# Kernel tuning notes

Measured on AMD Instinct MI355X. Metric: run time of the kernel, lower is better.

Reference implementation:

```python
import jax, jax.numpy as jnp
import numpy as np
from jax import lax

BS, K, N = 8, 8, 16            # batch, gathers per sample, picks per curve
T, WG = 3072, 64               # gather time samples, traces
H, WC = 256, 256               # CVEncoder ScaleSize
RH, RW = 1024, 512             # resize (also GatherEncoder outLen=RH)
T0, T1 = 0.0, 7000.0           # tInt[0], tInt[-1]


def setup_inputs() -> dict:
    key = jax.random.key(0)
    ks = jax.random.split(key, 8)
    gather = jax.random.normal(ks[0], (BS, K, T, WG), jnp.float32)
    # cv: times sorted, strictly > 0, within [T0, T1]; velocities within VMM range
    times = jnp.sort(jax.random.uniform(ks[1], (BS, K, N), minval=100.0, maxval=T1), axis=-1)
    vels = jnp.sort(jax.random.uniform(ks[2], (BS, K, N), minval=1500.0, maxval=4500.0), axis=-1)
    cv = jnp.stack([times, vels], axis=-1).astype(jnp.float32)
    VMM = jnp.tile(jnp.array([1500.0, 4500.0], jnp.float32), (BS, 1))
    def cw(k, shape):
        return (jax.random.normal(k, shape, jnp.float32) * 0.1)
    params = dict(
        w1=cw(ks[3], (1, 1, 3, 3)), b1=jnp.zeros((1,), jnp.float32), g1=jnp.ones((1,), jnp.float32), be1=jnp.zeros((1,), jnp.float32),
        w2=cw(ks[4], (2, 3, 3, 3)), b2=jnp.zeros((2,), jnp.float32), g2=jnp.ones((2,), jnp.float32), be2=jnp.zeros((2,), jnp.float32),
        w3=cw(ks[5], (1, 2, 3, 2)), b3=jnp.zeros((1,), jnp.float32), g3=jnp.ones((1,), jnp.float32), be3=jnp.zeros((1,), jnp.float32),
        wf=cw(ks[6], (1, 1, 3, 3)), bf=jnp.zeros((1,), jnp.float32), gf=jnp.ones((1,), jnp.float32), bef=jnp.zeros((1,), jnp.float32),
    )
    return {"gather": gather, "cv": cv, "VMM": VMM, **params}


def _conv(x, w, b, stride, pad):
    y = lax.conv_general_dilated(x, w, stride, pad, dimension_numbers=("NCHW", "OIHW", "NCHW"))
    return y + b[None, :, None, None]


def _bn(x, g, b, eps=1e-5):
    # training-mode BatchNorm2d: stats over (N, H, W)
    m = jnp.mean(x, (0, 2, 3), keepdims=True)
    v = jnp.var(x, (0, 2, 3), keepdims=True)
    return (x - m) / jnp.sqrt(v + eps) * g[None, :, None, None] + b[None, :, None, None]


def _lrelu(x):
    return jnp.where(x >= 0, x, 0.1 * x)


def _cbl(x, w, b, g, be, stride):
    return _lrelu(_bn(_conv(x, w, b, stride, "VALID"), g, be))


def _maxpool(x, k):
    p = k // 2
    return lax.reduce_window(x, -jnp.inf, lax.max, (1, 1, k, k), (1, 1, 1, 1),
                             ((0, 0), (0, 0), (p, p), (p, p)))


def _cv_mask(cv, VMM):
    # normalize times to fractional row index and velocities to fractional col index
    dt = (T1 - T0) / (H - 1)
    t_idx = (cv[..., 0] - T0) / dt                                        # (BS,K,N)
    dv = (VMM[:, 1] - VMM[:, 0]) / (WC - 1)                               # (BS,)
    v_idx = (cv[..., 1] - VMM[:, 0, None, None]) / dv[:, None, None]      # (BS,K,N)
    t_flat = t_idx.reshape(-1, N)
    v_flat = v_idx.reshape(-1, N)
    tq = jnp.arange(H, dtype=jnp.float32)
    # per-curve piecewise-linear interpolation of v over the time grid
    v_curve = jax.vmap(lambda xp, fp: jnp.interp(tq, xp, fp))(t_flat, v_flat)  # (M,H)
    v_int = jnp.clip(v_curve.astype(jnp.int32), 0, WC - 1)
    M = BS * K
    mask = jnp.full((M, H, WC), 0.01, jnp.float32)
    mask = mask.at[jnp.arange(M)[:, None], jnp.arange(H)[None, :], v_int].add(0.9)
    mask = mask.reshape(BS, K, H, WC)
    # bilinear resize, half-pixel centers == torch align_corners=False
    return jax.image.resize(mask, (BS, K, RH, RW), method="linear")


def _forward(gather, cv, VMM, w1, b1, g1, be1, w2, b2, g2, be2, w3, b3, g3, be3, wf, bf, gf, bef):
    cv_mask = lax.stop_gradient(_cv_mask(cv, VMM))          # CVEncoder runs under no_grad
    x = gather.reshape(-1, 1, T, WG)                        # (BS*K,1,T,WG)
    x = x / jnp.max(jnp.abs(x))                             # mode='mute': keep sign
    x = _cbl(x, w1, b1, g1, be1, (3, 2))                    # (M,1,1024,31)
    xcat = jnp.concatenate([x, _maxpool(x, 3), _maxpool(x, 5)], axis=1)
    x = _cbl(xcat, w2, b2, g2, be2, (3, 2))                 # (M,2,341,15)
    x = _cbl(x, w3, b3, g3, be3, (3, 2))                    # (M,1,113,7)
    x = jax.image.resize(x, (x.shape[0], 1, RH, 1), method="linear")
    genr = x.reshape(BS, K, RH, 1)
    mix = jnp.sum(genr * cv_mask, axis=1, keepdims=True)    # (BS,1,RH,RW)
    y = _conv(mix, wf, bf, (1, 1), ((1, 1), (1, 1)))
    return _lrelu(_bn(y, gf, bef))


def reference(gather, cv, VMM, w1, b1, g1, be1, w2, b2, g2, be2, w3, b3, g3, be3, wf, bf, gf, bef):
    return _forward(gather, cv, VMM, w1, b1, g1, be1, w2, b2, g2, be2, w3, b3, g3, be3, wf, bf, gf, bef)
```

## Files before the change

kernel.cpp:

```cpp
#include <hip/hip_runtime.h>
#include <math.h>

#define BSZ 8
#define KG  8
#define NP  16
#define MM  64
#define TT  3072
#define WGN 64
#define HH  256
#define WCN 256
#define RHN 1024
#define RWN 512

#define C1H 1024
#define C1W 31
#define C2H 341
#define C2W 15
#define C3H 113
#define C3W 7

#define N_GATHER (MM*TT*WGN)
#define N1 (MM*C1H*C1W)
#define N2 (MM*C2H*C2W)
#define N3 (MM*C3H*C3W)
#define NF (BSZ*RHN*RWN)

#define SL 8

#define OFF_AMAX 640
#define OFF_SCAL 672
#define OFF_VINT 768
#define OFF_Y1   (OFF_VINT + MM*HH*4)
#define OFF_Y2   (OFF_Y1  + N1*4)
#define OFF_Y3   (OFF_Y2  + 2*N2*4)
#define OFF_GENR (OFF_Y3  + N3*4)

__device__ __forceinline__ void blockAdd2(double s, double ss, double* o0, double* o1) {
    __shared__ double red[4][2];
    __syncthreads();
    int lane = threadIdx.x & 63, wid = threadIdx.x >> 6;
#pragma unroll
    for (int off = 32; off > 0; off >>= 1) {
        s  += __shfl_down(s,  off, 64);
        ss += __shfl_down(ss, off, 64);
    }
    if (lane == 0) { red[wid][0] = s; red[wid][1] = ss; }
    __syncthreads();
    if (threadIdx.x == 0) {
        double a = 0, b = 0;
        int nw = blockDim.x >> 6;
        for (int i = 0; i < nw; i++) { a += red[i][0]; b += red[i][1]; }
        int slot = blockIdx.x & (SL - 1);
        atomicAdd(&o0[slot], a); atomicAdd(&o1[slot], b);
    }
}

__global__ void k_absmax(const float* __restrict__ g, unsigned int* amax) {
    __shared__ float red[4];
    int tid = blockIdx.x * blockDim.x + threadIdx.x;
    int stride = gridDim.x * blockDim.x;
    const float4* g4 = (const float4*)g;
    float m = 0.f;
    for (int i = tid; i < N_GATHER / 4; i += stride) {
        float4 v = g4[i];
        m = fmaxf(m, fmaxf(fmaxf(fabsf(v.x), fabsf(v.y)), fmaxf(fabsf(v.z), fabsf(v.w))));
    }
#pragma unroll
    for (int off = 32; off > 0; off >>= 1) m = fmaxf(m, __shfl_down(m, off, 64));
    int lane = threadIdx.x & 63, wid = threadIdx.x >> 6;
    if (lane == 0) red[wid] = m;
    __syncthreads();
    if (threadIdx.x == 0) {
        float mm = fmaxf(fmaxf(red[0], red[1]), fmaxf(red[2], red[3]));
        atomicMax(&amax[blockIdx.x & (SL - 1)], __float_as_uint(mm));
    }
}

__global__ void k_conv1(const float* __restrict__ g, const float* __restrict__ w1,
                        const float* __restrict__ b1, const unsigned int* __restrict__ amax,
                        float* __restrict__ y1, double* sums) {
    float mx = 0.f;
#pragma unroll
    for (int i = 0; i < SL; i++) mx = fmaxf(mx, __uint_as_float(amax[i]));
    float inv = 1.0f / mx;
    float w[9];
#pragma unroll
    for (int i = 0; i < 9; i++) w[i] = w1[i] * inv;
    float bb = b1[0];
    double s = 0, ss = 0;
    int stride = gridDim.x * blockDim.x;
    for (int idx = blockIdx.x * blockDim.x + threadIdx.x; idx < N1; idx += stride) {
        int ow = idx % C1W;
        int t2 = idx / C1W;
        int oh = t2 % C1H;
        int m  = t2 / C1H;
        const float* xp = g + (size_t)m * TT * WGN + (size_t)(oh * 3) * WGN + ow * 2;
        float acc = bb;
#pragma unroll
        for (int r = 0; r < 3; r++)
#pragma unroll
            for (int c = 0; c < 3; c++) acc += w[r * 3 + c] * xp[r * WGN + c];
        y1[idx] = acc;
        s += acc; ss += (double)acc * (double)acc;
    }
    blockAdd2(s, ss, &sums[0], &sums[SL]);
}

__global__ void k_bnfin(const double* __restrict__ s, const float* __restrict__ g,
                        const float* __restrict__ be, float* __restrict__ ab,
                        int nch, double n) {
    int c = threadIdx.x;
    if (c < nch) {
        double sum = 0, sumsq = 0;
        for (int j = 0; j < SL; j++) {
            sum   += s[(2 * c) * SL + j];
            sumsq += s[(2 * c + 1) * SL + j];
        }
        double mean = sum / n;
        double var  = sumsq / n - mean * mean;
        double a = (double)g[c] / sqrt(var + 1e-5);
        ab[2 * c]     = (float)a;
        ab[2 * c + 1] = (float)((double)be[c] - mean * a);
    }
}

#define F2_OH 32
#define F2_NCH 11
#define F2_NRMAX (3*F2_OH + 4)
__global__ void k_fused2(const float* __restrict__ y1, const float* __restrict__ scal,
                         const float* __restrict__ w2, const float* __restrict__ b2,
                         float* __restrict__ y2, double* sums) {
    __shared__ float sact[F2_NRMAX][32];
    __shared__ float sr3[F2_NRMAX][32];
    __shared__ float sr5[F2_NRMAX][32];
    int m   = blockIdx.x / F2_NCH;
    int ch  = blockIdx.x % F2_NCH;
    int oh0 = ch * F2_OH;
    int OHa = min(F2_OH, C2H - oh0);
    int NR  = 3 * OHa + 4;
    int gl0 = 3 * oh0 - 2;
    float a1 = scal[0], b1 = scal[1];
    const float* yp = y1 + (size_t)m * C1H * C1W;
    for (int i = threadIdx.x; i < NR * C1W; i += blockDim.x) {
        int l = i / C1W, w = i % C1W;
        int gr = gl0 + l;
        float v = -INFINITY;
        if (gr >= 0 && gr < C1H) {
            v = a1 * yp[gr * C1W + w] + b1;
            v = v >= 0.f ? v : 0.1f * v;
        }
        sact[l][w] = v;
    }
    __syncthreads();
    for (int i = threadIdx.x; i < NR * C1W; i += blockDim.x) {
        int l = i / C1W, w = i % C1W;
        int wl1 = max(w - 1, 0), wr1 = min(w + 1, C1W - 1);
        int wl2 = max(w - 2, 0), wr2 = min(w + 2, C1W - 1);
        float c  = sact[l][w];
        float m3 = fmaxf(fmaxf(sact[l][wl1], c), sact[l][wr1]);
        float m5 = fmaxf(fmaxf(m3, sact[l][wl2]), sact[l][wr2]);
        sr3[l][w] = m3;
        sr5[l][w] = m5;
    }
    __syncthreads();
    double s0 = 0, ss0 = 0, s1 = 0, ss1 = 0;
    for (int o = threadIdx.x; o < OHa * C2W; o += blockDim.x) {
        int lo = o / C2W, ow = o % C2W;
        float a0 = b2[0], acc1 = b2[1];
#pragma unroll
        for (int i = 0; i < 3; i++) {
            int l = 3 * lo + 2 + i;
#pragma unroll
            for (int j = 0; j < 3; j++) {
                int wc = 2 * ow + j;
                float v0 = sact[l][wc];
                float v1 = fmaxf(fmaxf(sr3[l - 1][wc], sr3[l][wc]), sr3[l + 1][wc]);
                float v2 = fmaxf(fmaxf(fmaxf(sr5[l - 2][wc], sr5[l - 1][wc]), sr5[l][wc]),
                                 fmaxf(sr5[l + 1][wc], sr5[l + 2][wc]));
                int ki = i * 3 + j;
                a0   += w2[ki] * v0 + w2[9 + ki] * v1 + w2[18 + ki] * v2;
                acc1 += w2[27 + ki] * v0 + w2[36 + ki] * v1 + w2[45 + ki] * v2;
            }
        }
        size_t ob = (size_t)m * (2 * C2H * C2W) + (size_t)(oh0 + lo) * C2W + ow;
        y2[ob] = a0;
        y2[ob + C2H * C2W] = acc1;
        s0 += a0; ss0 += (double)a0 * a0;
        s1 += acc1; ss1 += (double)acc1 * acc1;
    }
    blockAdd2(s0, ss0, &sums[2 * SL], &sums[3 * SL]);
    blockAdd2(s1, ss1, &sums[4 * SL], &sums[5 * SL]);
}

__global__ void k_conv3(const float* __restrict__ y2, const float* __restrict__ scal,
                        const float* __restrict__ w3, const float* __restrict__ b3,
                        float* __restrict__ y3, double* sums) {
    double s = 0, ss = 0;
    float a20 = scal[2], b20 = scal[3], a21 = scal[4], b21 = scal[5];
    int stride = gridDim.x * blockDim.x;
    for (int idx = blockIdx.x * blockDim.x + threadIdx.x; idx < N3; idx += stride) {
        int ow = idx % C3W;
        int t2 = idx / C3W;
        int oh = t2 % C3H;
        int m  = t2 / C3H;
        float acc = b3[0];
#pragma unroll
        for (int i = 0; i < 2; i++) {
            float aa = i ? a21 : a20, bb = i ? b21 : b20;
            const float* cp = y2 + (size_t)m * (2 * C2H * C2W) + (size_t)i * C2H * C2W
                              + (size_t)(oh * 3) * C2W + ow * 2;
#pragma unroll
            for (int r = 0; r < 3; r++)
#pragma unroll
                for (int c = 0; c < 2; c++) {
                    float v = aa * cp[r * C2W + c] + bb;
                    v = v >= 0.f ? v : 0.1f * v;
                    acc += w3[i * 6 + r * 2 + c] * v;
                }
        }
        y3[idx] = acc;
        s += acc; ss += (double)acc * acc;
    }
    blockAdd2(s, ss, &sums[6 * SL], &sums[7 * SL]);
}

__global__ void k_vint(const float* __restrict__ cv, const float* __restrict__ VMM,
                       int* __restrict__ vint) {
    __shared__ float tt[NP], vv[NP];
    int m = blockIdx.x;
    int b = m >> 3;
    if (threadIdx.x < NP) {
        int n = threadIdx.x;
        float t = cv[(m * NP + n) * 2 + 0];
        float v = cv[(m * NP + n) * 2 + 1];
        float dt = 7000.0f / 255.0f;
        tt[n] = t / dt;
        float vmin = VMM[b * 2], vmax = VMM[b * 2 + 1];
        float dv = (vmax - vmin) / 255.0f;
        vv[n] = (v - vmin) / dv;
    }
    __syncthreads();
    int h = threadIdx.x;
    float x = (float)h;
    float val;
    if (x <= tt[0]) val = vv[0];
    else if (x >= tt[NP - 1]) val = vv[NP - 1];
    else {
        int i = 1;
        while (i < NP - 1 && tt[i] <= x) i++;
        float d = tt[i] - tt[i - 1];
        val = (d != 0.f) ? vv[i - 1] + (x - tt[i - 1]) / d * (vv[i] - vv[i - 1]) : vv[i];
    }
    int vi = (int)val;
    vi = max(0, min(WCN - 1, vi));
    vint[m * HH + h] = vi;
}

__global__ void k_genr(const float* __restrict__ y3, const float* __restrict__ scal,
                       float* __restrict__ genr) {
    __shared__ float tile[C3H * C3W];
    int m = blockIdx.x;
    float a = scal[6], b = scal[7];
    for (int i = threadIdx.x; i < C3H * C3W; i += blockDim.x) {
        float v = a * y3[m * C3H * C3W + i] + b;
        tile[i] = v >= 0.f ? v : 0.1f * v;
    }
    __syncthreads();
    const float cw0 = 4.f / 37.f, cw1 = 5.f / 37.f, cw2 = 6.f / 37.f, cw3 = 7.f / 37.f;
    const float cw[7] = { cw0, cw1, cw2, cw3, cw2, cw1, cw0 };
    for (int i = threadIdx.x; i < RHN; i += blockDim.x) {
        float sh = (i + 0.5f) * (113.0f / 1024.0f) - 0.5f;
        float fl = floorf(sh);
        float fr = sh - fl;
        int i0 = (int)fl, i1 = i0 + 1;
        i0 = max(0, min(C3H - 1, i0));
        i1 = max(0, min(C3H - 1, i1));
        float acc = 0.f;
#pragma unroll
        for (int x = 0; x < 7; x++) {
            float v = (1.f - fr) * tile[i0 * C3W + x] + fr * tile[i1 * C3W + x];
            acc += cw[x] * v;
        }
        genr[m * RHN + i] = acc;
    }
}

#define MC_TH 16
__global__ void k_mixconvf(const float* __restrict__ genr, const int* __restrict__ vint,
                           const float* __restrict__ wf, const float* __restrict__ bf,
                           float* __restrict__ out, double* sums) {
    __shared__ float tile[MC_TH + 2][RWN + 2];
    __shared__ float Grow[MC_TH + 2];
    int b  = blockIdx.x / (RHN / MC_TH);
    int chk = blockIdx.x % (RHN / MC_TH);
    int h0 = chk * MC_TH;
    for (int i = threadIdx.x; i < (MC_TH + 2) * (RWN + 2); i += blockDim.x)
        ((float*)tile)[i] = 0.f;
    if (threadIdx.x < MC_TH + 2) Grow[threadIdx.x] = 0.f;
    __syncthreads();
    if (threadIdx.x < (MC_TH + 2) * KG) {
        int r = threadIdx.x / KG, k = threadIdx.x % KG;
        int h = h0 - 1 + r;
        if (h >= 0 && h < RHN) {
            int m = b * KG + k;
            float g = genr[m * RHN + h];
            atomicAdd(&Grow[r], g);
            float sh = (h + 0.5f) * 0.25f - 0.5f;
            float fl = floorf(sh);
            float fh = sh - fl;
            int ih0 = (int)fl, ih1 = ih0 + 1;
            ih0 = max(0, min(HH - 1, ih0));
            ih1 = max(0, min(HH - 1, ih1));
            int vv[2] = { vint[m * HH + ih0], vint[m * HH + ih1] };
            float aa[2] = { 0.9f * g * (1.f - fh), 0.9f * g * fh };
#pragma unroll
            for (int t = 0; t < 2; t++) {
                int v = vv[t]; float A = aa[t];
                if (v == 0) {
                    atomicAdd(&tile[r][1 + 0], A);
                    atomicAdd(&tile[r][1 + 1], 0.75f * A);
                    atomicAdd(&tile[r][1 + 2], 0.25f * A);
                } else if (v == WCN - 1) {
                    atomicAdd(&tile[r][1 + 509], 0.25f * A);
                    atomicAdd(&tile[r][1 + 510], 0.75f * A);
                    atomicAdd(&tile[r][1 + 511], A);
                } else {
                    atomicAdd(&tile[r][1 + 2 * v - 1], 0.25f * A);
                    atomicAdd(&tile[r][1 + 2 * v],     0.75f * A);
                    atomicAdd(&tile[r][1 + 2 * v + 1], 0.75f * A);
                    atomicAdd(&tile[r][1 + 2 * v + 2], 0.25f * A);
                }
            }
        }
    }
    __syncthreads();
    for (int i = threadIdx.x; i < (MC_TH + 2) * RWN; i += blockDim.x) {
        int r = i / RWN, w = i % RWN;
        int h = h0 - 1 + r;
        if (h >= 0 && h < RHN) tile[r][w + 1] += 0.01f * Grow[r];
    }
    __syncthreads();
    float w[9];
#pragma unroll
    for (int i = 0; i < 9; i++) w[i] = wf[i];
    float bb = bf[0];
    double s = 0, ss = 0;
    for (int o = threadIdx.x; o < MC_TH * RWN; o += blockDim.x) {
        int lr = o / RWN, x = o % RWN;
        float acc = bb;
#pragma unroll
        for (int dr = 0; dr < 3; dr++)
#pragma unroll
            for (int dc = 0; dc < 3; dc++)
                acc += w[dr * 3 + dc] * tile[lr + dr][x + dc];
        out[((size_t)b * RHN + (h0 + lr)) * RWN + x] = acc;
        s += acc; ss += (double)acc * acc;
    }
    blockAdd2(s, ss, &sums[8 * SL], &sums[9 * SL]);
}

__global__ void k_act4(float4* __restrict__ x, const float* __restrict__ ab, int n4) {
    int i = blockIdx.x * blockDim.x + threadIdx.x;
    if (i < n4) {
        float a = ab[0], b = ab[1];
        float4 v = x[i];
        v.x = a * v.x + b; v.x = v.x >= 0.f ? v.x : 0.1f * v.x;
        v.y = a * v.y + b; v.y = v.y >= 0.f ? v.y : 0.1f * v.y;
        v.z = a * v.z + b; v.z = v.z >= 0.f ? v.z : 0.1f * v.z;
        v.w = a * v.w + b; v.w = v.w >= 0.f ? v.w : 0.1f * v.w;
        x[i] = v;
    }
}

extern "C" void kernel_launch(void* const* d_in, const int* in_sizes, int n_in,
                              void* d_out, int out_size, void* d_ws, size_t ws_size,
                              hipStream_t stream) {
    const float* gather = (const float*)d_in[0];
    const float* cv     = (const float*)d_in[1];
    const float* VMM    = (const float*)d_in[2];
    const float* w1 = (const float*)d_in[3];
    const float* b1 = (const float*)d_in[4];
    const float* g1 = (const float*)d_in[5];
    const float* be1 = (const float*)d_in[6];
    const float* w2 = (const float*)d_in[7];
    const float* b2 = (const float*)d_in[8];
    const float* g2 = (const float*)d_in[9];
    const float* be2 = (const float*)d_in[10];
    const float* w3 = (const float*)d_in[11];
    const float* b3 = (const float*)d_in[12];
    const float* g3 = (const float*)d_in[13];
    const float* be3 = (const float*)d_in[14];
    const float* wf = (const float*)d_in[15];
    const float* bf = (const float*)d_in[16];
    const float* gf = (const float*)d_in[17];
    const float* bef = (const float*)d_in[18];
    float* out = (float*)d_out;

    char* ws = (char*)d_ws;
    double* sums        = (double*)ws;
    unsigned int* amax  = (unsigned int*)(ws + OFF_AMAX);
    float* scal         = (float*)(ws + OFF_SCAL);
    int*   vint         = (int*)(ws + OFF_VINT);
    float* y1           = (float*)(ws + OFF_Y1);
    float* y2           = (float*)(ws + OFF_Y2);
    float* y3           = (float*)(ws + OFF_Y3);
    float* genr         = (float*)(ws + OFF_GENR);

    hipMemsetAsync(d_ws, 0, 768, stream);

    k_absmax<<<512, 256, 0, stream>>>(gather, amax);
    k_conv1<<<512, 256, 0, stream>>>(gather, w1, b1, amax, y1, sums);
    k_bnfin<<<1, 64, 0, stream>>>(sums + 0, g1, be1, scal + 0, 1, (double)N1);
    k_fused2<<<MM * F2_NCH, 256, 0, stream>>>(y1, scal, w2, b2, y2, sums);
    k_bnfin<<<1, 64, 0, stream>>>(sums + 2 * SL, g2, be2, scal + 2, 2, (double)N2);
    k_conv3<<<198, 256, 0, stream>>>(y2, scal, w3, b3, y3, sums);
    k_bnfin<<<1, 64, 0, stream>>>(sums + 6 * SL, g3, be3, scal + 6, 1, (double)N3);
    k_vint<<<MM, 256, 0, stream>>>(cv, VMM, vint);
    k_genr<<<MM, 256, 0, stream>>>(y3, scal, genr);
    k_mixconvf<<<BSZ * (RHN / MC_TH), 256, 0, stream>>>(genr, vint, wf, bf, out, sums);
    k_bnfin<<<1, 64, 0, stream>>>(sums + 8 * SL, gf, bef, scal + 8, 1, (double)NF);
    k_act4<<<(NF / 4 + 255) / 256, 256, 0, stream>>>((float4*)out, scal + 8, NF / 4);
}
```

Baseline: 205.8 us.

## Drop absmax pass via BN scale invariance, fold BN finalize into consumers

Removes the global abs-max reduction over the gather tensor. Training-mode BatchNorm after conv1 cancels any uniform input scaling, apart from the small eps term, so that pass is redundant. The separate BN-finalize kernels are replaced by an inline helper that each consumer kernel runs from the atomic sums. The final in-place activation pass is removed by splitting the mix/conv stage into a statistics pass and a second pass that recomputes the tile and writes the normalized, activated output directly. This trades extra compute in the mix stage for fewer launches and less full-tensor memory traffic.

```diff
diff --git a/kernel.cpp b/kernel.cpp
--- a/kernel.cpp
+++ b/kernel.cpp
@@ -19,7 +19,6 @@
 #define C3H 113
 #define C3W 7
 
-#define N_GATHER (MM*TT*WGN)
 #define N1 (MM*C1H*C1W)
 #define N2 (MM*C2H*C2W)
 #define N3 (MM*C3H*C3W)
@@ -27,8 +26,6 @@
 
 #define SL 8
 
-#define OFF_AMAX 640
-#define OFF_SCAL 672
 #define OFF_VINT 768
 #define OFF_Y1   (OFF_VINT + MM*HH*4)
 #define OFF_Y2   (OFF_Y1  + N1*4)
@@ -55,37 +52,27 @@
     }
 }
 
-__global__ void k_absmax(const float* __restrict__ g, unsigned int* amax) {
-    __shared__ float red[4];
-    int tid = blockIdx.x * blockDim.x + threadIdx.x;
-    int stride = gridDim.x * blockDim.x;
-    const float4* g4 = (const float4*)g;
-    float m = 0.f;
-    for (int i = tid; i < N_GATHER / 4; i += stride) {
-        float4 v = g4[i];
-        m = fmaxf(m, fmaxf(fmaxf(fabsf(v.x), fabsf(v.y)), fmaxf(fabsf(v.z), fabsf(v.w))));
-    }
-#pragma unroll
-    for (int off = 32; off > 0; off >>= 1) m = fmaxf(m, __shfl_down(m, off, 64));
-    int lane = threadIdx.x & 63, wid = threadIdx.x >> 6;
-    if (lane == 0) red[wid] = m;
-    __syncthreads();
-    if (threadIdx.x == 0) {
-        float mm = fmaxf(fmaxf(red[0], red[1]), fmaxf(red[2], red[3]));
-        atomicMax(&amax[blockIdx.x & (SL - 1)], __float_as_uint(mm));
-    }
+__device__ __forceinline__ float2 bn_ab(const double* __restrict__ sums, int c,
+                                        const float* __restrict__ g,
+                                        const float* __restrict__ be, double n) {
+    double sum = 0, sumsq = 0;
+#pragma unroll
+    for (int j = 0; j < SL; j++) {
+        sum   += sums[(2 * c) * SL + j];
+        sumsq += sums[(2 * c + 1) * SL + j];
+    }
+    double mean = sum / n;
+    double var  = sumsq / n - mean * mean;
+    double a = (double)g[c] / sqrt(var + 1e-5);
+    return make_float2((float)a, (float)((double)be[c] - mean * a));
 }
 
 __global__ void k_conv1(const float* __restrict__ g, const float* __restrict__ w1,
-                        const float* __restrict__ b1, const unsigned int* __restrict__ amax,
+                        const float* __restrict__ b1,
                         float* __restrict__ y1, double* sums) {
-    float mx = 0.f;
-#pragma unroll
-    for (int i = 0; i < SL; i++) mx = fmaxf(mx, __uint_as_float(amax[i]));
-    float inv = 1.0f / mx;
     float w[9];
 #pragma unroll
-    for (int i = 0; i < 9; i++) w[i] = w1[i] * inv;
+    for (int i = 0; i < 9; i++) w[i] = w1[i];
     float bb = b1[0];
     double s = 0, ss = 0;
     int stride = gridDim.x * blockDim.x;
@@ -106,47 +93,30 @@
     blockAdd2(s, ss, &sums[0], &sums[SL]);
 }
 
-__global__ void k_bnfin(const double* __restrict__ s, const float* __restrict__ g,
-                        const float* __restrict__ be, float* __restrict__ ab,
-                        int nch, double n) {
-    int c = threadIdx.x;
-    if (c < nch) {
-        double sum = 0, sumsq = 0;
-        for (int j = 0; j < SL; j++) {
-            sum   += s[(2 * c) * SL + j];
-            sumsq += s[(2 * c + 1) * SL + j];
-        }
-        double mean = sum / n;
-        double var  = sumsq / n - mean * mean;
-        double a = (double)g[c] / sqrt(var + 1e-5);
-        ab[2 * c]     = (float)a;
-        ab[2 * c + 1] = (float)((double)be[c] - mean * a);
-    }
-}
-
 #define F2_OH 32
 #define F2_NCH 11
 #define F2_NRMAX (3*F2_OH + 4)
-__global__ void k_fused2(const float* __restrict__ y1, const float* __restrict__ scal,
+__global__ void k_fused2(const float* __restrict__ y1, const double* __restrict__ sums_r,
+                         const float* __restrict__ g1, const float* __restrict__ be1,
                          const float* __restrict__ w2, const float* __restrict__ b2,
                          float* __restrict__ y2, double* sums) {
     __shared__ float sact[F2_NRMAX][32];
     __shared__ float sr3[F2_NRMAX][32];
     __shared__ float sr5[F2_NRMAX][32];
+    float2 ab1 = bn_ab(sums_r, 0, g1, be1, (double)N1);
     int m   = blockIdx.x / F2_NCH;
     int ch  = blockIdx.x % F2_NCH;
     int oh0 = ch * F2_OH;
     int OHa = min(F2_OH, C2H - oh0);
     int NR  = 3 * OHa + 4;
     int gl0 = 3 * oh0 - 2;
-    float a1 = scal[0], b1 = scal[1];
     const float* yp = y1 + (size_t)m * C1H * C1W;
     for (int i = threadIdx.x; i < NR * C1W; i += blockDim.x) {
         int l = i / C1W, w = i % C1W;
         int gr = gl0 + l;
         float v = -INFINITY;
         if (gr >= 0 && gr < C1H) {
-            v = a1 * yp[gr * C1W + w] + b1;
+            v = ab1.x * yp[gr * C1W + w] + ab1.y;
             v = v >= 0.f ? v : 0.1f * v;
         }
         sact[l][w] = v;
@@ -192,11 +162,13 @@
     blockAdd2(s1, ss1, &sums[4 * SL], &sums[5 * SL]);
 }
 
-__global__ void k_conv3(const float* __restrict__ y2, const float* __restrict__ scal,
+__global__ void k_conv3(const float* __restrict__ y2, const double* __restrict__ sums_r,
+                        const float* __restrict__ g2, const float* __restrict__ be2,
                         const float* __restrict__ w3, const float* __restrict__ b3,
                         float* __restrict__ y3, double* sums) {
+    float2 ab20 = bn_ab(sums_r + 2 * SL, 0, g2, be2, (double)N2);
+    float2 ab21 = bn_ab(sums_r + 2 * SL, 1, g2, be2, (double)N2);
     double s = 0, ss = 0;
-    float a20 = scal[2], b20 = scal[3], a21 = scal[4], b21 = scal[5];
     int stride = gridDim.x * blockDim.x;
     for (int idx = blockIdx.x * blockDim.x + threadIdx.x; idx < N3; idx += stride) {
         int ow = idx % C3W;
@@ -206,7 +178,7 @@
         float acc = b3[0];
 #pragma unroll
         for (int i = 0; i < 2; i++) {
-            float aa = i ? a21 : a20, bb = i ? b21 : b20;
+            float aa = i ? ab21.x : ab20.x, bb = i ? ab21.y : ab20.y;
             const float* cp = y2 + (size_t)m * (2 * C2H * C2W) + (size_t)i * C2H * C2W
                               + (size_t)(oh * 3) * C2W + ow * 2;
 #pragma unroll
@@ -224,11 +196,15 @@
     blockAdd2(s, ss, &sums[6 * SL], &sums[7 * SL]);
 }
 
-__global__ void k_vint(const float* __restrict__ cv, const float* __restrict__ VMM,
-                       int* __restrict__ vint) {
+__global__ void k_vintgenr(const float* __restrict__ cv, const float* __restrict__ VMM,
+                           const float* __restrict__ y3, const double* __restrict__ sums_r,
+                           const float* __restrict__ g3, const float* __restrict__ be3,
+                           int* __restrict__ vint, float* __restrict__ genr) {
     __shared__ float tt[NP], vv[NP];
+    __shared__ float tile[C3H * C3W];
     int m = blockIdx.x;
     int b = m >> 3;
+    float2 ab3 = bn_ab(sums_r + 6 * SL, 0, g3, be3, (double)N3);
     if (threadIdx.x < NP) {
         int n = threadIdx.x;
         float t = cv[(m * NP + n) * 2 + 0];
@@ -239,33 +215,26 @@
         float dv = (vmax - vmin) / 255.0f;
         vv[n] = (v - vmin) / dv;
     }
-    __syncthreads();
-    int h = threadIdx.x;
-    float x = (float)h;
-    float val;
-    if (x <= tt[0]) val = vv[0];
-    else if (x >= tt[NP - 1]) val = vv[NP - 1];
-    else {
-        int i = 1;
-        while (i < NP - 1 && tt[i] <= x) i++;
-        float d = tt[i] - tt[i - 1];
-        val = (d != 0.f) ? vv[i - 1] + (x - tt[i - 1]) / d * (vv[i] - vv[i - 1]) : vv[i];
-    }
-    int vi = (int)val;
-    vi = max(0, min(WCN - 1, vi));
-    vint[m * HH + h] = vi;
-}
-
-__global__ void k_genr(const float* __restrict__ y3, const float* __restrict__ scal,
-                       float* __restrict__ genr) {
-    __shared__ float tile[C3H * C3W];
-    int m = blockIdx.x;
-    float a = scal[6], b = scal[7];
     for (int i = threadIdx.x; i < C3H * C3W; i += blockDim.x) {
-        float v = a * y3[m * C3H * C3W + i] + b;
+        float v = ab3.x * y3[m * C3H * C3W + i] + ab3.y;
         tile[i] = v >= 0.f ? v : 0.1f * v;
     }
     __syncthreads();
+    {
+        int h = threadIdx.x;
+        float x = (float)h;
+        float val;
+        if (x <= tt[0]) val = vv[0];
+        else if (x >= tt[NP - 1]) val = vv[NP - 1];
+        else {
+            int i = 1;
+            while (i < NP - 1 && tt[i] <= x) i++;
+            float d = tt[i] - tt[i - 1];
+            val = (d != 0.f) ? vv[i - 1] + (x - tt[i - 1]) / d * (vv[i] - vv[i - 1]) : vv[i];
+        }
+        int vi = (int)val;
+        vint[m * HH + h] = max(0, min(WCN - 1, vi));
+    }
     const float cw0 = 4.f / 37.f, cw1 = 5.f / 37.f, cw2 = 6.f / 37.f, cw3 = 7.f / 37.f;
     const float cw[7] = { cw0, cw1, cw2, cw3, cw2, cw1, cw0 };
     for (int i = threadIdx.x; i < RHN; i += blockDim.x) {
@@ -286,14 +255,10 @@
 }
 
 #define MC_TH 16
-__global__ void k_mixconvf(const float* __restrict__ genr, const int* __restrict__ vint,
-                           const float* __restrict__ wf, const float* __restrict__ bf,
-                           float* __restrict__ out, double* sums) {
-    __shared__ float tile[MC_TH + 2][RWN + 2];
-    __shared__ float Grow[MC_TH + 2];
-    int b  = blockIdx.x / (RHN / MC_TH);
-    int chk = blockIdx.x % (RHN / MC_TH);
-    int h0 = chk * MC_TH;
+__device__ __forceinline__ void build_mix_tile(const float* __restrict__ genr,
+                                               const int* __restrict__ vint,
+                                               int b, int h0,
+                                               float (*tile)[RWN + 2], float* Grow) {
     for (int i = threadIdx.x; i < (MC_TH + 2) * (RWN + 2); i += blockDim.x)
         ((float*)tile)[i] = 0.f;
     if (threadIdx.x < MC_TH + 2) Grow[threadIdx.x] = 0.f;
@@ -340,6 +305,16 @@
         if (h >= 0 && h < RHN) tile[r][w + 1] += 0.01f * Grow[r];
     }
     __syncthreads();
+}
+
+__global__ void k_mixA(const float* __restrict__ genr, const int* __restrict__ vint,
+                       const float* __restrict__ wf, const float* __restrict__ bf,
+                       double* sums) {
+    __shared__ float tile[MC_TH + 2][RWN + 2];
+    __shared__ float Grow[MC_TH + 2];
+    int b   = blockIdx.x / (RHN / MC_TH);
+    int h0  = (blockIdx.x % (RHN / MC_TH)) * MC_TH;
+    build_mix_tile(genr, vint, b, h0, tile, Grow);
     float w[9];
 #pragma unroll
     for (int i = 0; i < 9; i++) w[i] = wf[i];
@@ -353,22 +328,35 @@
 #pragma unroll
             for (int dc = 0; dc < 3; dc++)
                 acc += w[dr * 3 + dc] * tile[lr + dr][x + dc];
-        out[((size_t)b * RHN + (h0 + lr)) * RWN + x] = acc;
         s += acc; ss += (double)acc * acc;
     }
     blockAdd2(s, ss, &sums[8 * SL], &sums[9 * SL]);
 }
 
-__global__ void k_act4(float4* __restrict__ x, const float* __restrict__ ab, int n4) {
-    int i = blockIdx.x * blockDim.x + threadIdx.x;
-    if (i < n4) {
-        float a = ab[0], b = ab[1];
-        float4 v = x[i];
-        v.x = a * v.x + b; v.x = v.x >= 0.f ? v.x : 0.1f * v.x;
-        v.y = a * v.y + b; v.y = v.y >= 0.f ? v.y : 0.1f * v.y;
-        v.z = a * v.z + b; v.z = v.z >= 0.f ? v.z : 0.1f * v.z;
-        v.w = a * v.w + b; v.w = v.w >= 0.f ? v.w : 0.1f * v.w;
-        x[i] = v;
+__global__ void k_mixB(const float* __restrict__ genr, const int* __restrict__ vint,
+                       const float* __restrict__ wf, const float* __restrict__ bf,
+                       const double* __restrict__ sums_r, const float* __restrict__ gf,
+                       const float* __restrict__ bef, float* __restrict__ out) {
+    __shared__ float tile[MC_TH + 2][RWN + 2];
+    __shared__ float Grow[MC_TH + 2];
+    float2 abf = bn_ab(sums_r + 8 * SL, 0, gf, bef, (double)NF);
+    int b   = blockIdx.x / (RHN / MC_TH);
+    int h0  = (blockIdx.x % (RHN / MC_TH)) * MC_TH;
+    build_mix_tile(genr, vint, b, h0, tile, Grow);
+    float w[9];
+#pragma unroll
+    for (int i = 0; i < 9; i++) w[i] = wf[i];
+    float bb = bf[0];
+    for (int o = threadIdx.x; o < MC_TH * RWN; o += blockDim.x) {
+        int lr = o / RWN, x = o % RWN;
+        float acc = bb;
+#pragma unroll
+        for (int dr = 0; dr < 3; dr++)
+#pragma unroll
+            for (int dc = 0; dc < 3; dc++)
+                acc += w[dr * 3 + dc] * tile[lr + dr][x + dc];
+        float v = abf.x * acc + abf.y;
+        out[((size_t)b * RHN + (h0 + lr)) * RWN + x] = v >= 0.f ? v : 0.1f * v;
     }
 }
 
@@ -397,27 +385,19 @@
     float* out = (float*)d_out;
 
     char* ws = (char*)d_ws;
-    double* sums        = (double*)ws;
-    unsigned int* amax  = (unsigned int*)(ws + OFF_AMAX);
-    float* scal         = (float*)(ws + OFF_SCAL);
-    int*   vint         = (int*)(ws + OFF_VINT);
-    float* y1           = (float*)(ws + OFF_Y1);
-    float* y2           = (float*)(ws + OFF_Y2);
-    float* y3           = (float*)(ws + OFF_Y3);
-    float* genr         = (float*)(ws + OFF_GENR);
-
-    hipMemsetAsync(d_ws, 0, 768, stream);
-
-    k_absmax<<<512, 256, 0, stream>>>(gather, amax);
-    k_conv1<<<512, 256, 0, stream>>>(gather, w1, b1, amax, y1, sums);
-    k_bnfin<<<1, 64, 0, stream>>>(sums + 0, g1, be1, scal + 0, 1, (double)N1);
-    k_fused2<<<MM * F2_NCH, 256, 0, stream>>>(y1, scal, w2, b2, y2, sums);
-    k_bnfin<<<1, 64, 0, stream>>>(sums + 2 * SL, g2, be2, scal + 2, 2, (double)N2);
-    k_conv3<<<198, 256, 0, stream>>>(y2, scal, w3, b3, y3, sums);
-    k_bnfin<<<1, 64, 0, stream>>>(sums + 6 * SL, g3, be3, scal + 6, 1, (double)N3);
-    k_vint<<<MM, 256, 0, stream>>>(cv, VMM, vint);
-    k_genr<<<MM, 256, 0, stream>>>(y3, scal, genr);
-    k_mixconvf<<<BSZ * (RHN / MC_TH), 256, 0, stream>>>(genr, vint, wf, bf, out, sums);
-    k_bnfin<<<1, 64, 0, stream>>>(sums + 8 * SL, gf, bef, scal + 8, 1, (double)NF);
-    k_act4<<<(NF / 4 + 255) / 256, 256, 0, stream>>>((float4*)out, scal + 8, NF / 4);
-}
+    double* sums = (double*)ws;
+    int*   vint  = (int*)(ws + OFF_VINT);
+    float* y1    = (float*)(ws + OFF_Y1);
+    float* y2    = (float*)(ws + OFF_Y2);
+    float* y3    = (float*)(ws + OFF_Y3);
+    float* genr  = (float*)(ws + OFF_GENR);
+
+    hipMemsetAsync(d_ws, 0, 640, stream);
+
+    k_conv1<<<512, 256, 0, stream>>>(gather, w1, b1, y1, sums);
+    k_fused2<<<MM * F2_NCH, 256, 0, stream>>>(y1, sums, g1, be1, w2, b2, y2, sums);
+    k_conv3<<<198, 256, 0, stream>>>(y2, sums, g2, be2, w3, b3, y3, sums);
+    k_vintgenr<<<MM, 256, 0, stream>>>(cv, VMM, y3, sums, g3, be3, vint, genr);
+    k_mixA<<<BSZ * (RHN / MC_TH), 256, 0, stream>>>(genr, vint, wf, bf, sums);
+    k_mixB<<<BSZ * (RHN / MC_TH), 256, 0, stream>>>(genr, vint, wf, bf, sums, gf, bef, out);
+}
```

Measured after the change: 196.9 us, median of 2. 4.3% less time.
